# Kernel tuning notes

Measured on AMD Instinct MI355X. Metric: run time of the kernel, lower is better.

Reference implementation:

```python
import jax, jax.numpy as jnp
import numpy as np

HEADS = 8
DIM_KEY = 256
NUM_KEYS = 256           # sqrt(num_experts)
PK_TOPK = 16             # product_key_topk (defaults to num_experts_per_head)
K_PER_HEAD = 16          # num_experts_per_head


def setup_inputs() -> dict:
    key = jax.random.key(0)
    k1, k2, k3, k4, k5 = jax.random.split(key, 5)
    b, n, d = 2, 1024, 512          # batch MUST be 2 (see module quirk)
    num_experts = NUM_KEYS * NUM_KEYS
    x = jax.random.normal(k1, (b, n, d), jnp.float32)
    Wq = jax.random.normal(k2, (2 * HEADS * DIM_KEY, d), jnp.float32) * 0.02
    keys = jax.random.normal(k3, (HEADS, NUM_KEYS, 2, DIM_KEY), jnp.float32)
    w_down = jax.random.normal(k4, (num_experts, d), jnp.float32) * 0.02
    w_up = jax.random.normal(k5, (num_experts, d), jnp.float32) * 0.02
    return {"x": x, "Wq": Wq, "keys": keys, "w_down": w_down, "w_up": w_up}


def reference(x, Wq, keys, w_down, w_up):
    b, n, d = x.shape  # b == 2 required by the original module's einsum/unpack
    # to_queries: Linear -> Unflatten(-1,(2,h,dk)) -> permute(0,2,1,3,4)
    q = (x @ Wq.T).reshape(b, n, 2, HEADS, DIM_KEY).transpose(0, 2, 1, 3, 4)  # (b,2,n,h,dk)
    kk = keys.transpose(2, 0, 1, 3)  # (2, h, num_keys, dk)
    # faithful to original: 'p' axis of queries is the BATCH axis (requires b==2)
    sim = jnp.einsum('pbnhd,phkd->pbnhk', q, kk)  # (2, 2, n, h, num_keys)
    sx, ix = jax.lax.top_k(sim[0], PK_TOPK)
    sy, iy = jax.lax.top_k(sim[1], PK_TOPK)
    # combine product keys: (2, n, h, T, T) -> (2, n, h, T*T)
    all_scores = (sx[..., :, None] + sy[..., None, :]).reshape(*sx.shape[:-1], PK_TOPK * PK_TOPK)
    all_indices = (ix[..., :, None] * NUM_KEYS + iy[..., None, :]).reshape(*ix.shape[:-1], PK_TOPK * PK_TOPK)
    scores, pk = jax.lax.top_k(all_scores, K_PER_HEAD)          # (2, n, h, K)
    indices = jnp.take_along_axis(all_indices, pk, axis=-1)     # (2, n, h, K)
    wd = w_down[indices]  # (2, n, h, K, d) huge gather
    wu = w_up[indices]    # (2, n, h, K, d)
    h = jnp.einsum('bnd,bnhkd->bnhk', x, wd)
    h = jax.nn.gelu(h, approximate=False)  # torch nn.GELU default = exact erf
    h = h * jax.nn.softmax(scores, axis=-1)
    return jnp.einsum('bnhk,bnhkd->bnd', h, wu)
```

## Files before the change

### kernel.cpp

```cpp
#include <hip/hip_runtime.h>
#include <hip/hip_bf16.h>
#include <math.h>

__device__ __forceinline__ unsigned f2u(float f) {
    unsigned b = __float_as_uint(f);
    return b ^ ((unsigned)((int)b >> 31) | 0x80000000u);
}
__device__ __forceinline__ float u2f(unsigned u) {
    unsigned b = (u & 0x80000000u) ? (u ^ 0x80000000u) : ~u;
    return __uint_as_float(b);
}
__device__ __forceinline__ unsigned short f2bf(float f) {
    unsigned b = __float_as_uint(f);
    return (unsigned short)((b + 0x7FFFu + ((b >> 16) & 1u)) >> 16);
}
__device__ __forceinline__ float bflo(unsigned u) { return __uint_as_float(u << 16); }
__device__ __forceinline__ float bfhi(unsigned u) { return __uint_as_float(u & 0xFFFF0000u); }

__device__ __forceinline__ void radix16(unsigned u0, unsigned u1, unsigned u2, unsigned u3,
                                        unsigned& T, int& kk) {
    unsigned prefix = 0; int k = 16;
    for (int b = 31; b >= 0; --b) {
        unsigned hi = (prefix >> b) | 1u;
        int cnt = __popcll(__ballot((u0 >> b) == hi))
                + __popcll(__ballot((u1 >> b) == hi))
                + __popcll(__ballot((u2 >> b) == hi))
                + __popcll(__ballot((u3 >> b) == hi));
        if (cnt >= k) prefix |= (1u << b); else k -= cnt;
    }
    T = prefix; kk = k;
}

__global__ __launch_bounds__(256) void k_conv(const float* __restrict__ src,
                                              unsigned short* __restrict__ dst, int n8) {
    int tid = blockIdx.x * 256 + threadIdx.x;
    int stride = gridDim.x * 256;
    for (int i = tid; i < n8; i += stride) {
        float4 a = *(const float4*)&src[(size_t)i * 8];
        float4 b = *(const float4*)&src[(size_t)i * 8 + 4];
        uint4 o;
        o.x = (unsigned)f2bf(a.x) | ((unsigned)f2bf(a.y) << 16);
        o.y = (unsigned)f2bf(a.z) | ((unsigned)f2bf(a.w) << 16);
        o.z = (unsigned)f2bf(b.x) | ((unsigned)f2bf(b.y) << 16);
        o.w = (unsigned)f2bf(b.z) | ((unsigned)f2bf(b.w) << 16);
        *(uint4*)&dst[(size_t)i * 8] = o;
    }
}

__global__ __launch_bounds__(256) void kK2(const float* __restrict__ keys,
                                           const float* __restrict__ Wq,
                                           float* __restrict__ K2) {
    __shared__ float As[16][128];
    __shared__ float Bs[16][128];
    int t  = threadIdx.x;
    int tx = t & 15, ty = t >> 4;
    int p = blockIdx.z;
    int ktile = blockIdx.y & 1, ch = blockIdx.y >> 1;
    int h = ch & 7, c = ch >> 3;
    int m0 = ktile * 128;
    int n0 = blockIdx.x * 128;
    const float* kb = keys + ((size_t)(h * 256 + m0) * 2 + p) * 256;
    const float* wb = Wq + (size_t)(c * 2048 + h * 256) * 512;
    float acc[8][8] = {};
    for (int k0 = 0; k0 < 256; k0 += 16) {
#pragma unroll
        for (int i = 0; i < 2; ++i) {
            int u   = t * 2 + i;
            int row = u >> 2;
            int kc  = (u & 3) << 2;
            float4 av = *(const float4*)&kb[(size_t)row * 512 + k0 + kc];
            As[kc + 0][row] = av.x; As[kc + 1][row] = av.y; As[kc + 2][row] = av.z; As[kc + 3][row] = av.w;
            int v = u;
            int dkrow = v >> 5;
            int dcol  = (v & 31) << 2;
            float4 bv = *(const float4*)&wb[(size_t)(k0 + dkrow) * 512 + n0 + dcol];
            *(float4*)&Bs[dkrow][dcol] = bv;
        }
        __syncthreads();
#pragma unroll
        for (int kk = 0; kk < 16; ++kk) {
            float4 a0 = *(const float4*)&As[kk][ty * 8];
            float4 a1 = *(const float4*)&As[kk][ty * 8 + 4];
            float4 b0 = *(const float4*)&Bs[kk][tx * 4];
            float4 b1 = *(const float4*)&Bs[kk][tx * 4 + 64];
            float a[8] = {a0.x, a0.y, a0.z, a0.w, a1.x, a1.y, a1.z, a1.w};
            float b[8] = {b0.x, b0.y, b0.z, b0.w, b1.x, b1.y, b1.z, b1.w};
#pragma unroll
            for (int i = 0; i < 8; ++i)
#pragma unroll
                for (int j = 0; j < 8; ++j) acc[i][j] += a[i] * b[j];
        }
        __syncthreads();
    }
    float* Cp = K2 + (size_t)p * 4096 * 512;
#pragma unroll
    for (int i = 0; i < 8; ++i) {
        int r = c * 2048 + h * 256 + m0 + ty * 8 + i;
        float4 o0; o0.x = acc[i][0]; o0.y = acc[i][1]; o0.z = acc[i][2]; o0.w = acc[i][3];
        float4 o1; o1.x = acc[i][4]; o1.y = acc[i][5]; o1.z = acc[i][6]; o1.w = acc[i][7];
        *(float4*)&Cp[(size_t)r * 512 + n0 + tx * 4]      = o0;
        *(float4*)&Cp[(size_t)r * 512 + n0 + 64 + tx * 4] = o1;
    }
}

__global__ __launch_bounds__(256) void kS_gemm(const float* __restrict__ x,
                                               const float* __restrict__ K2,
                                               float* __restrict__ S) {
    __shared__ float As[16][128];
    __shared__ float Bs[16][128];
    int t  = threadIdx.x;
    int tx = t & 15, ty = t >> 4;
    int p  = blockIdx.z;
    int m0 = blockIdx.y * 128, n0 = blockIdx.x * 128;
    const float* A = x  + (size_t)p * 1024 * 512;
    const float* B = K2 + (size_t)p * 4096 * 512;
    float* C = S + (size_t)p * 1024 * 4096;
    float acc[8][8] = {};
    for (int k0 = 0; k0 < 512; k0 += 16) {
#pragma unroll
        for (int i = 0; i < 2; ++i) {
            int u   = t * 2 + i;
            int row = u >> 2;
            int kc  = (u & 3) << 2;
            float4 av = *(const float4*)&A[(size_t)(m0 + row) * 512 + k0 + kc];
            float4 bv = *(const float4*)&B[(size_t)(n0 + row) * 512 + k0 + kc];
            As[kc + 0][row] = av.x; As[kc + 1][row] = av.y; As[kc + 2][row] = av.z; As[kc + 3][row] = av.w;
            Bs[kc + 0][row] = bv.x; Bs[kc + 1][row] = bv.y; Bs[kc + 2][row] = bv.z; Bs[kc + 3][row] = bv.w;
        }
        __syncthreads();
#pragma unroll
        for (int kk = 0; kk < 16; ++kk) {
            float4 a0 = *(const float4*)&As[kk][ty * 8];
            float4 a1 = *(const float4*)&As[kk][ty * 8 + 4];
            float4 b0 = *(const float4*)&Bs[kk][tx * 4];
            float4 b1 = *(const float4*)&Bs[kk][tx * 4 + 64];
            float a[8] = {a0.x, a0.y, a0.z, a0.w, a1.x, a1.y, a1.z, a1.w};
            float b[8] = {b0.x, b0.y, b0.z, b0.w, b1.x, b1.y, b1.z, b1.w};
#pragma unroll
            for (int i = 0; i < 8; ++i)
#pragma unroll
                for (int j = 0; j < 8; ++j) acc[i][j] += a[i] * b[j];
        }
        __syncthreads();
    }
#pragma unroll
    for (int i = 0; i < 8; ++i) {
        int m = m0 + ty * 8 + i;
        float4 o0; o0.x = acc[i][0]; o0.y = acc[i][1]; o0.z = acc[i][2]; o0.w = acc[i][3];
        float4 o1; o1.x = acc[i][4]; o1.y = acc[i][5]; o1.z = acc[i][6]; o1.w = acc[i][7];
        *(float4*)&C[(size_t)m * 4096 + n0 + tx * 4]      = o0;
        *(float4*)&C[(size_t)m * 4096 + n0 + 64 + tx * 4] = o1;
    }
}

__global__ __launch_bounds__(256) void k2_topk(const float* __restrict__ S,
                                               int* __restrict__ widx,
                                               float* __restrict__ wcoef) {
    __shared__ float sx_s[4][2][16];
    __shared__ int   ix_s[4][2][16];

    int t = threadIdx.x;
    int wv = t >> 6, ln = t & 63;
    int task = blockIdx.x * 4 + wv;
    int c = task >> 13;
    int n = (task >> 3) & 1023;
    int h = task & 7;
    unsigned long long lt = (1ull << ln) - 1ull;

    const float* s0p = S + (size_t)n * 4096 + c * 2048 + h * 256 + ln * 4;
    float4 s0 = *(const float4*)&s0p[0];
    float4 s1 = *(const float4*)&s0p[1024UL * 4096];

#define TK_HALF(PIDX, V)                                                          \
    {                                                                             \
        unsigned u0 = f2u(V.x), u1 = f2u(V.y), u2 = f2u(V.z), u3 = f2u(V.w);      \
        unsigned T; int kk;                                                       \
        radix16(u0, u1, u2, u3, T, kk);                                           \
        int base = 0;                                                             \
        { unsigned long long m = __ballot(u0 > T);                                \
          if (u0 > T) { int pos = base + __popcll(m & lt);                        \
              sx_s[wv][PIDX][pos] = V.x; ix_s[wv][PIDX][pos] = ln * 4 + 0; }      \
          base += __popcll(m); }                                                  \
        { unsigned long long m = __ballot(u1 > T);                                \
          if (u1 > T) { int pos = base + __popcll(m & lt);                        \
              sx_s[wv][PIDX][pos] = V.y; ix_s[wv][PIDX][pos] = ln * 4 + 1; }      \
          base += __popcll(m); }                                                  \
        { unsigned long long m = __ballot(u2 > T);                                \
          if (u2 > T) { int pos = base + __popcll(m & lt);                        \
              sx_s[wv][PIDX][pos] = V.z; ix_s[wv][PIDX][pos] = ln * 4 + 2; }      \
          base += __popcll(m); }                                                  \
        { unsigned long long m = __ballot(u3 > T);                                \
          if (u3 > T) { int pos = base + __popcll(m & lt);                        \
              sx_s[wv][PIDX][pos] = V.w; ix_s[wv][PIDX][pos] = ln * 4 + 3; }      \
          base += __popcll(m); }                                                  \
        { unsigned long long m = __ballot(u0 == T); int r = __popcll(m & lt);     \
          if ((u0 == T) && r < kk) { sx_s[wv][PIDX][base + r] = V.x;              \
              ix_s[wv][PIDX][base + r] = ln * 4 + 0; }                            \
          int cn2 = __popcll(m); int tk = cn2 < kk ? cn2 : kk; base += tk; kk -= tk; } \
        { unsigned long long m = __ballot(u1 == T); int r = __popcll(m & lt);     \
          if ((u1 == T) && r < kk) { sx_s[wv][PIDX][base + r] = V.y;              \
              ix_s[wv][PIDX][base + r] = ln * 4 + 1; }                            \
          int cn2 = __popcll(m); int tk = cn2 < kk ? cn2 : kk; base += tk; kk -= tk; } \
        { unsigned long long m = __ballot(u2 == T); int r = __popcll(m & lt);     \
          if ((u2 == T) && r < kk) { sx_s[wv][PIDX][base + r] = V.z;              \
              ix_s[wv][PIDX][base + r] = ln * 4 + 2; }                            \
          int cn2 = __popcll(m); int tk = cn2 < kk ? cn2 : kk; base += tk; kk -= tk; } \
        { unsigned long long m = __ballot(u3 == T); int r = __popcll(m & lt);     \
          if ((u3 == T) && r < kk) { sx_s[wv][PIDX][base + r] = V.w;              \
              ix_s[wv][PIDX][base + r] = ln * 4 + 3; }                            \
          int cn2 = __popcll(m); int tk = cn2 < kk ? cn2 : kk; base += tk; kk -= tk; } \
    }
    TK_HALF(0, s0);
    TK_HALF(1, s1);
#undef TK_HALF
    __syncthreads();

    int t0 = ln, t1 = ln + 64, t2 = ln + 128, t3 = ln + 192;
    float vc0 = sx_s[wv][0][t0 >> 4] + sx_s[wv][1][t0 & 15];
    float vc1 = sx_s[wv][0][t1 >> 4] + sx_s[wv][1][t1 & 15];
    float vc2 = sx_s[wv][0][t2 >> 4] + sx_s[wv][1][t2 & 15];
    float vc3 = sx_s[wv][0][t3 >> 4] + sx_s[wv][1][t3 & 15];
    unsigned u0 = f2u(vc0), u1 = f2u(vc1), u2 = f2u(vc2), u3 = f2u(vc3);
    unsigned T; int kk;
    radix16(u0, u1, u2, u3, T, kk);
    float Tf = u2f(T);

    bool w0 = u0 > T, w1 = u1 > T, w2 = u2 > T, w3 = u3 > T;
    int q0 = 0, q1 = 0, q2 = 0, q3 = 0;
    int base = 0;
    { unsigned long long m = __ballot(w0); q0 = base + __popcll(m & lt); base += __popcll(m); }
    { unsigned long long m = __ballot(w1); q1 = base + __popcll(m & lt); base += __popcll(m); }
    { unsigned long long m = __ballot(w2); q2 = base + __popcll(m & lt); base += __popcll(m); }
    { unsigned long long m = __ballot(w3); q3 = base + __popcll(m & lt); base += __popcll(m); }
#define CMB_EQ(UJ, WJ, QJ) { unsigned long long m = __ballot(UJ == T);          \
    int r = __popcll(m & lt);                                                   \
    if ((UJ == T) && r < kk) { WJ = true; QJ = base + r; }                      \
    int cn2 = __popcll(m); int tk = cn2 < kk ? cn2 : kk;                        \
    base += tk; kk -= tk; }
    CMB_EQ(u0, w0, q0); CMB_EQ(u1, w1, q1); CMB_EQ(u2, w2, q2); CMB_EQ(u3, w3, q3);
#undef CMB_EQ

    float e0 = 0.f, e1 = 0.f, e2 = 0.f, e3 = 0.f;
    int id0 = 0, id1 = 0, id2 = 0, id3 = 0;
    float es = 0.f;
    if (w0) { e0 = __expf(vc0 - Tf); es += e0; id0 = ix_s[wv][0][t0 >> 4] * 256 + ix_s[wv][1][t0 & 15]; }
    if (w1) { e1 = __expf(vc1 - Tf); es += e1; id1 = ix_s[wv][0][t1 >> 4] * 256 + ix_s[wv][1][t1 & 15]; }
    if (w2) { e2 = __expf(vc2 - Tf); es += e2; id2 = ix_s[wv][0][t2 >> 4] * 256 + ix_s[wv][1][t2 & 15]; }
    if (w3) { e3 = __expf(vc3 - Tf); es += e3; id3 = ix_s[wv][0][t3 >> 4] * 256 + ix_s[wv][1][t3 & 15]; }
    for (int s = 1; s < 64; s <<= 1) es += __shfl_xor(es, s);
    float inv = 1.f / es;

    int off = ((c * 1024 + n) * 8 + h) * 16;
    if (w0) { wcoef[off + q0] = e0 * inv; widx[off + q0] = id0; }
    if (w1) { wcoef[off + q1] = e1 * inv; widx[off + q1] = id1; }
    if (w2) { wcoef[off + q2] = e2 * inv; widx[off + q2] = id2; }
    if (w3) { wcoef[off + q3] = e3 * inv; widx[off + q3] = id3; }
}

__global__ __launch_bounds__(256) void k3_experts_bf16(const float* __restrict__ x,
                                                       const unsigned short* __restrict__ wd,
                                                       const unsigned short* __restrict__ wu,
                                                       const int* __restrict__ widx,
                                                       const float* __restrict__ wcoef,
                                                       float* __restrict__ out) {
    int bid = blockIdx.x;
    int c = bid >> 10, n = bid & 1023;
    int t = threadIdx.x, wv = t >> 6, ln = t & 63;
    __shared__ float wacc[4][512];

    const float* xrow = &x[(c * 1024 + n) * 512];
    float xr[8], oacc[8];
    {
        float4 xa = *(const float4*)&xrow[ln * 8];
        float4 xb = *(const float4*)&xrow[ln * 8 + 4];
        xr[0] = xa.x; xr[1] = xa.y; xr[2] = xa.z; xr[3] = xa.w;
        xr[4] = xb.x; xr[5] = xb.y; xr[6] = xb.z; xr[7] = xb.w;
    }
#pragma unroll
    for (int j = 0; j < 8; ++j) oacc[j] = 0.f;

    const int base = (c * 1024 + n) * 128;
    for (int e = wv * 32; e < wv * 32 + 32; ++e) {
        int   idx = widx[base + e];
        float wgt = wcoef[base + e];
        uint4 dv = *(const uint4*)&wd[(size_t)idx * 512 + ln * 8];
        float part = bflo(dv.x) * xr[0] + bfhi(dv.x) * xr[1]
                   + bflo(dv.y) * xr[2] + bfhi(dv.y) * xr[3]
                   + bflo(dv.z) * xr[4] + bfhi(dv.z) * xr[5]
                   + bflo(dv.w) * xr[6] + bfhi(dv.w) * xr[7];
        for (int s = 1; s < 64; s <<= 1) part += __shfl_xor(part, s);
        float hv = part;
        float coef = 0.5f * hv * (1.f + erff(hv * 0.70710678118654752f)) * wgt;
        uint4 uv = *(const uint4*)&wu[(size_t)idx * 512 + ln * 8];
        oacc[0] += coef * bflo(uv.x); oacc[1] += coef * bfhi(uv.x);
        oacc[2] += coef * bflo(uv.y); oacc[3] += coef * bfhi(uv.y);
        oacc[4] += coef * bflo(uv.z); oacc[5] += coef * bfhi(uv.z);
        oacc[6] += coef * bflo(uv.w); oacc[7] += coef * bfhi(uv.w);
    }

#pragma unroll
    for (int j = 0; j < 8; ++j) wacc[wv][ln * 8 + j] = oacc[j];
    __syncthreads();

    float* orow = &out[(c * 1024 + n) * 512];
    for (int d = t; d < 512; d += 256)
        orow[d] = wacc[0][d] + wacc[1][d] + wacc[2][d] + wacc[3][d];
}

__global__ __launch_bounds__(256) void k3_experts_f32(const float* __restrict__ x,
                                                      const float* __restrict__ w_down,
                                                      const float* __restrict__ w_up,
                                                      const int* __restrict__ widx,
                                                      const float* __restrict__ wcoef,
                                                      float* __restrict__ out) {
    int bid = blockIdx.x;
    int c = bid >> 10, n = bid & 1023;
    int t = threadIdx.x, wv = t >> 6, ln = t & 63;
    __shared__ float wacc[4][512];

    const float* xrow = &x[(c * 1024 + n) * 512];
    float xr[8], oacc[8];
    {
        float4 xa = *(const float4*)&xrow[ln * 8];
        float4 xb = *(const float4*)&xrow[ln * 8 + 4];
        xr[0] = xa.x; xr[1] = xa.y; xr[2] = xa.z; xr[3] = xa.w;
        xr[4] = xb.x; xr[5] = xb.y; xr[6] = xb.z; xr[7] = xb.w;
    }
#pragma unroll
    for (int j = 0; j < 8; ++j) oacc[j] = 0.f;

    const int base = (c * 1024 + n) * 128;
    for (int e = wv * 32; e < wv * 32 + 32; ++e) {
        int   idx = widx[base + e];
        float wgt = wcoef[base + e];
        const float* dr = &w_down[(long)idx * 512 + ln * 8];
        float4 da = *(const float4*)&dr[0];
        float4 db = *(const float4*)&dr[4];
        float part = da.x * xr[0] + da.y * xr[1] + da.z * xr[2] + da.w * xr[3]
                   + db.x * xr[4] + db.y * xr[5] + db.z * xr[6] + db.w * xr[7];
        for (int s = 1; s < 64; s <<= 1) part += __shfl_xor(part, s);
        float hv = part;
        float coef = 0.5f * hv * (1.f + erff(hv * 0.70710678118654752f)) * wgt;
        const float* ur = &w_up[(long)idx * 512 + ln * 8];
        float4 ua = *(const float4*)&ur[0];
        float4 ub = *(const float4*)&ur[4];
        oacc[0] += coef * ua.x; oacc[1] += coef * ua.y; oacc[2] += coef * ua.z; oacc[3] += coef * ua.w;
        oacc[4] += coef * ub.x; oacc[5] += coef * ub.y; oacc[6] += coef * ub.z; oacc[7] += coef * ub.w;
    }
#pragma unroll
    for (int j = 0; j < 8; ++j) wacc[wv][ln * 8 + j] = oacc[j];
    __syncthreads();

    float* orow = &out[(c * 1024 + n) * 512];
    for (int d = t; d < 512; d += 256)
        orow[d] = wacc[0][d] + wacc[1][d] + wacc[2][d] + wacc[3][d];
}

extern "C" void kernel_launch(void* const* d_in, const int* in_sizes, int n_in,
                              void* d_out, int out_size, void* d_ws, size_t ws_size,
                              hipStream_t stream) {
    const float* x      = (const float*)d_in[0];
    const float* Wq     = (const float*)d_in[1];
    const float* keys   = (const float*)d_in[2];
    const float* w_down = (const float*)d_in[3];
    const float* w_up   = (const float*)d_in[4];
    float* out = (float*)d_out;

    char* ws = (char*)d_ws;
    size_t off = 0;
    float* S     = (float*)(ws + off); off += 2048UL * 4096 * 4;
    int*   widx  = (int*)(ws + off);   off += 262144UL * 4;
    float* wcoef = (float*)(ws + off); off += 262144UL * 4;
    float* K2    = (float*)(ws + off); off += 2UL * 4096 * 512 * 4;
    unsigned short* wd16 = (unsigned short*)(ws + off); off += 65536UL * 512 * 2;
    unsigned short* wu16 = (unsigned short*)(ws + off); off += 65536UL * 512 * 2;
    bool use_bf16 = (ws_size >= off);

    kK2<<<dim3(4, 32, 2), 256, 0, stream>>>(keys, Wq, K2);
    kS_gemm<<<dim3(32, 8, 2), 256, 0, stream>>>(x, K2, S);
    k2_topk<<<4096, 256, 0, stream>>>(S, widx, wcoef);
    if (use_bf16) {
        k_conv<<<2048, 256, 0, stream>>>(w_down, wd16, 65536 * 512 / 8);
        k_conv<<<2048, 256, 0, stream>>>(w_up,   wu16, 65536 * 512 / 8);
        k3_experts_bf16<<<2048, 256, 0, stream>>>(x, wd16, wu16, widx, wcoef, out);
    } else {
        k3_experts_f32<<<2048, 256, 0, stream>>>(x, w_down, w_up, widx, wcoef, out);
    }
}
```

Baseline: 345.4 us.

## Compute similarity GEMM with bf16 MFMA instead of fp32 FMA tiles

Converts x to bf16 and makes the K2 projection emit bf16. The similarity GEMM that feeds top-k now runs on 16x16x32 bf16 MFMA instructions, loading operands directly from global memory with no shared-memory staging. This targets the cost of the fp32 SIMT GEMM that produces S. The trade-off is lower precision in the similarity scores, which could change which experts top-k selects, plus one extra conversion launch.

```diff
diff --git a/kernel.cpp b/kernel.cpp
--- a/kernel.cpp
+++ b/kernel.cpp
@@ -1,6 +1,9 @@
 #include <hip/hip_runtime.h>
 #include <hip/hip_bf16.h>
 #include <math.h>
+
+typedef __attribute__((ext_vector_type(8))) short bf16x8;
+typedef __attribute__((ext_vector_type(4))) float f32x4;
 
 __device__ __forceinline__ unsigned f2u(float f) {
     unsigned b = __float_as_uint(f);
@@ -49,7 +52,7 @@
 
 __global__ __launch_bounds__(256) void kK2(const float* __restrict__ keys,
                                            const float* __restrict__ Wq,
-                                           float* __restrict__ K2) {
+                                           unsigned short* __restrict__ K2b) {
     __shared__ float As[16][128];
     __shared__ float Bs[16][128];
     int t  = threadIdx.x;
@@ -92,65 +95,65 @@
         }
         __syncthreads();
     }
-    float* Cp = K2 + (size_t)p * 4096 * 512;
+    unsigned short* Cp = K2b + (size_t)p * 4096 * 512;
 #pragma unroll
     for (int i = 0; i < 8; ++i) {
         int r = c * 2048 + h * 256 + m0 + ty * 8 + i;
-        float4 o0; o0.x = acc[i][0]; o0.y = acc[i][1]; o0.z = acc[i][2]; o0.w = acc[i][3];
-        float4 o1; o1.x = acc[i][4]; o1.y = acc[i][5]; o1.z = acc[i][6]; o1.w = acc[i][7];
-        *(float4*)&Cp[(size_t)r * 512 + n0 + tx * 4]      = o0;
-        *(float4*)&Cp[(size_t)r * 512 + n0 + 64 + tx * 4] = o1;
-    }
-}
-
-__global__ __launch_bounds__(256) void kS_gemm(const float* __restrict__ x,
-                                               const float* __restrict__ K2,
+        uint2 o0, o1;
+        o0.x = (unsigned)f2bf(acc[i][0]) | ((unsigned)f2bf(acc[i][1]) << 16);
+        o0.y = (unsigned)f2bf(acc[i][2]) | ((unsigned)f2bf(acc[i][3]) << 16);
+        o1.x = (unsigned)f2bf(acc[i][4]) | ((unsigned)f2bf(acc[i][5]) << 16);
+        o1.y = (unsigned)f2bf(acc[i][6]) | ((unsigned)f2bf(acc[i][7]) << 16);
+        *(uint2*)&Cp[(size_t)r * 512 + n0 + tx * 4]      = o0;
+        *(uint2*)&Cp[(size_t)r * 512 + n0 + 64 + tx * 4] = o1;
+    }
+}
+
+__global__ __launch_bounds__(256) void kS_mfma(const unsigned short* __restrict__ xb,
+                                               const unsigned short* __restrict__ k2b,
                                                float* __restrict__ S) {
-    __shared__ float As[16][128];
-    __shared__ float Bs[16][128];
-    int t  = threadIdx.x;
-    int tx = t & 15, ty = t >> 4;
+    int t = threadIdx.x;
+    int wv = t >> 6, ln = t & 63;
     int p  = blockIdx.z;
-    int m0 = blockIdx.y * 128, n0 = blockIdx.x * 128;
-    const float* A = x  + (size_t)p * 1024 * 512;
-    const float* B = K2 + (size_t)p * 4096 * 512;
+    int n0 = blockIdx.y * 128 + wv * 32;
+    int e0 = blockIdx.x * 64;
+    const unsigned short* A = xb  + (size_t)p * 1024 * 512;
+    const unsigned short* B = k2b + (size_t)p * 4096 * 512;
+    int lr = ln & 15;
+    int lk = (ln >> 4) * 8;
+
+    f32x4 acc00 = {}, acc01 = {}, acc02 = {}, acc03 = {};
+    f32x4 acc10 = {}, acc11 = {}, acc12 = {}, acc13 = {};
+
+    for (int k0 = 0; k0 < 512; k0 += 32) {
+        bf16x8 a0 = *(const bf16x8*)&A[(size_t)(n0 + lr) * 512 + k0 + lk];
+        bf16x8 a1 = *(const bf16x8*)&A[(size_t)(n0 + 16 + lr) * 512 + k0 + lk];
+        bf16x8 b0 = *(const bf16x8*)&B[(size_t)(e0 + lr) * 512 + k0 + lk];
+        bf16x8 b1 = *(const bf16x8*)&B[(size_t)(e0 + 16 + lr) * 512 + k0 + lk];
+        bf16x8 b2 = *(const bf16x8*)&B[(size_t)(e0 + 32 + lr) * 512 + k0 + lk];
+        bf16x8 b3 = *(const bf16x8*)&B[(size_t)(e0 + 48 + lr) * 512 + k0 + lk];
+        acc00 = __builtin_amdgcn_mfma_f32_16x16x32_bf16(a0, b0, acc00, 0, 0, 0);
+        acc01 = __builtin_amdgcn_mfma_f32_16x16x32_bf16(a0, b1, acc01, 0, 0, 0);
+        acc02 = __builtin_amdgcn_mfma_f32_16x16x32_bf16(a0, b2, acc02, 0, 0, 0);
+        acc03 = __builtin_amdgcn_mfma_f32_16x16x32_bf16(a0, b3, acc03, 0, 0, 0);
+        acc10 = __builtin_amdgcn_mfma_f32_16x16x32_bf16(a1, b0, acc10, 0, 0, 0);
+        acc11 = __builtin_amdgcn_mfma_f32_16x16x32_bf16(a1, b1, acc11, 0, 0, 0);
+        acc12 = __builtin_amdgcn_mfma_f32_16x16x32_bf16(a1, b2, acc12, 0, 0, 0);
+        acc13 = __builtin_amdgcn_mfma_f32_16x16x32_bf16(a1, b3, acc13, 0, 0, 0);
+    }
+
     float* C = S + (size_t)p * 1024 * 4096;
-    float acc[8][8] = {};
-    for (int k0 = 0; k0 < 512; k0 += 16) {
-#pragma unroll
-        for (int i = 0; i < 2; ++i) {
-            int u   = t * 2 + i;
-            int row = u >> 2;
-            int kc  = (u & 3) << 2;
-            float4 av = *(const float4*)&A[(size_t)(m0 + row) * 512 + k0 + kc];
-            float4 bv = *(const float4*)&B[(size_t)(n0 + row) * 512 + k0 + kc];
-            As[kc + 0][row] = av.x; As[kc + 1][row] = av.y; As[kc + 2][row] = av.z; As[kc + 3][row] = av.w;
-            Bs[kc + 0][row] = bv.x; Bs[kc + 1][row] = bv.y; Bs[kc + 2][row] = bv.z; Bs[kc + 3][row] = bv.w;
-        }
-        __syncthreads();
-#pragma unroll
-        for (int kk = 0; kk < 16; ++kk) {
-            float4 a0 = *(const float4*)&As[kk][ty * 8];
-            float4 a1 = *(const float4*)&As[kk][ty * 8 + 4];
-            float4 b0 = *(const float4*)&Bs[kk][tx * 4];
-            float4 b1 = *(const float4*)&Bs[kk][tx * 4 + 64];
-            float a[8] = {a0.x, a0.y, a0.z, a0.w, a1.x, a1.y, a1.z, a1.w};
-            float b[8] = {b0.x, b0.y, b0.z, b0.w, b1.x, b1.y, b1.z, b1.w};
-#pragma unroll
-            for (int i = 0; i < 8; ++i)
-#pragma unroll
-                for (int j = 0; j < 8; ++j) acc[i][j] += a[i] * b[j];
-        }
-        __syncthreads();
-    }
-#pragma unroll
-    for (int i = 0; i < 8; ++i) {
-        int m = m0 + ty * 8 + i;
-        float4 o0; o0.x = acc[i][0]; o0.y = acc[i][1]; o0.z = acc[i][2]; o0.w = acc[i][3];
-        float4 o1; o1.x = acc[i][4]; o1.y = acc[i][5]; o1.z = acc[i][6]; o1.w = acc[i][7];
-        *(float4*)&C[(size_t)m * 4096 + n0 + tx * 4]      = o0;
-        *(float4*)&C[(size_t)m * 4096 + n0 + 64 + tx * 4] = o1;
-    }
+    int rbase = (ln >> 4) * 4;
+    int cw = ln & 15;
+#define STORE_FRAG(ACC, AF, BF)                                                   \
+    {                                                                             \
+        _Pragma("unroll")                                                         \
+        for (int r = 0; r < 4; ++r)                                               \
+            C[(size_t)(n0 + (AF)*16 + rbase + r) * 4096 + e0 + (BF)*16 + cw] = ACC[r]; \
+    }
+    STORE_FRAG(acc00, 0, 0); STORE_FRAG(acc01, 0, 1); STORE_FRAG(acc02, 0, 2); STORE_FRAG(acc03, 0, 3);
+    STORE_FRAG(acc10, 1, 0); STORE_FRAG(acc11, 1, 1); STORE_FRAG(acc12, 1, 2); STORE_FRAG(acc13, 1, 3);
+#undef STORE_FRAG
 }
 
 __global__ __launch_bounds__(256) void k2_topk(const float* __restrict__ S,
@@ -371,13 +374,15 @@
     float* S     = (float*)(ws + off); off += 2048UL * 4096 * 4;
     int*   widx  = (int*)(ws + off);   off += 262144UL * 4;
     float* wcoef = (float*)(ws + off); off += 262144UL * 4;
-    float* K2    = (float*)(ws + off); off += 2UL * 4096 * 512 * 4;
+    unsigned short* K2b = (unsigned short*)(ws + off); off += 2UL * 4096 * 512 * 2;
+    unsigned short* xb  = (unsigned short*)(ws + off); off += 2048UL * 512 * 2;
     unsigned short* wd16 = (unsigned short*)(ws + off); off += 65536UL * 512 * 2;
     unsigned short* wu16 = (unsigned short*)(ws + off); off += 65536UL * 512 * 2;
     bool use_bf16 = (ws_size >= off);
 
-    kK2<<<dim3(4, 32, 2), 256, 0, stream>>>(keys, Wq, K2);
-    kS_gemm<<<dim3(32, 8, 2), 256, 0, stream>>>(x, K2, S);
+    k_conv<<<512, 256, 0, stream>>>(x, xb, 2048 * 512 / 8);
+    kK2<<<dim3(4, 32, 2), 256, 0, stream>>>(keys, Wq, K2b);
+    kS_mfma<<<dim3(64, 8, 2), 256, 0, stream>>>(xb, K2b, S);
     k2_topk<<<4096, 256, 0, stream>>>(S, widx, wcoef);
     if (use_bf16) {
         k_conv<<<2048, 256, 0, stream>>>(w_down, wd16, 65536 * 512 / 8);
```

New measurement: 294.4 us. 1.17x faster.
